# Performance work log

Measured on AMD Instinct MI355X. Metric: run time of the kernel, lower is better.

## Reference

```python
import jax, jax.numpy as jnp
import numpy as np

START_ID = 0  # vocab.wd_to_id['<START>']

B, T, V = 128, 256, 1000
C = H = E = 512          # context_size == hidden_size (hidden initialized to context)
IN = C + E               # LSTMCell input size


def setup_inputs() -> dict:
    key = jax.random.key(0)
    ks = jax.random.split(key, 10)
    s = 1.0 / np.sqrt(H)
    return {
        "context": jax.random.normal(ks[0], (B, C), dtype=jnp.float32),
        "target_tensor": jax.random.randint(ks[1], (B, T), 0, V),
        "coin": jax.random.uniform(ks[2], (T,), dtype=jnp.float32),
        "embed_table": jax.random.normal(ks[3], (V, E), dtype=jnp.float32) * 0.02,
        "W_ih": jax.random.uniform(ks[4], (4 * H, IN), dtype=jnp.float32, minval=-s, maxval=s),
        "W_hh": jax.random.uniform(ks[5], (4 * H, H), dtype=jnp.float32, minval=-s, maxval=s),
        "b_ih": jax.random.uniform(ks[6], (4 * H,), dtype=jnp.float32, minval=-s, maxval=s),
        "b_hh": jax.random.uniform(ks[7], (4 * H,), dtype=jnp.float32, minval=-s, maxval=s),
        "W_out": jax.random.uniform(ks[8], (V, H), dtype=jnp.float32, minval=-s, maxval=s),
        "b_out": jax.random.uniform(ks[9], (V,), dtype=jnp.float32, minval=-s, maxval=s),
    }


def reference(context, target_tensor, coin, embed_table, W_ih, W_hh, b_ih, b_hh, W_out, b_out):
    Bsz, Csz = context.shape
    Tlen = target_tensor.shape[1]
    Hsz = W_hh.shape[1]
    Vsz = W_out.shape[0]

    # teacher token for step i is target[:, i-1]; step 0 uses START
    prev_tok = jnp.concatenate(
        [jnp.full((Bsz, 1), START_ID, dtype=target_tensor.dtype), target_tensor[:, :-1]],
        axis=1,
    ).T  # (T, B)

    h0 = context                                   # hidden initialized to context
    c0 = jnp.zeros((Bsz, Hsz), dtype=context.dtype)
    logits0 = jnp.zeros((Bsz, Vsz), dtype=context.dtype)
    steps = jnp.arange(Tlen)

    def step(carry, xs):
        h, c, prev_logits = carry
        tok, r, i = xs
        greedy = jnp.argmax(prev_logits, axis=1)               # previous prediction
        idx = jnp.where(r > 0.5, tok, jnp.where(i == 0, START_ID, greedy))
        emb = embed_table[idx]                                 # (B, E)
        x = jnp.concatenate([context, emb], axis=1)            # (B, C+E)
        gates = x @ W_ih.T + b_ih + h @ W_hh.T + b_hh          # (B, 4H)
        ig, fg, gg, og = jnp.split(gates, 4, axis=1)           # torch order i,f,g,o
        c_new = jax.nn.sigmoid(fg) * c + jax.nn.sigmoid(ig) * jnp.tanh(gg)
        h_new = jax.nn.sigmoid(og) * jnp.tanh(c_new)
        logits = h_new @ W_out.T + b_out                       # (B, V)
        return (h_new, c_new, logits), logits

    (h, c, _), outs = jax.lax.scan(step, (h0, c0, logits0), (prev_tok, coin, steps))
    return outs.transpose(1, 0, 2), h, c  # (B, T, V), (B, H), (B, H)
```

## Files before the change

### kernel.cpp

```cpp
#include <hip/hip_runtime.h>
#include <cstdint>
#include <cstddef>

#define B_SZ 128
#define T_SZ 256
#define V_SZ 1000
#define H_SZ 512
#define NG   2048
#define VP   1024

typedef unsigned long long u64;

__device__ __forceinline__ unsigned fkey(float f) {
  unsigned u = __float_as_uint(f);
  return (u & 0x80000000u) ? ~u : (u | 0x80000000u);
}
__device__ __forceinline__ float sigf(float x) { return 1.0f / (1.0f + expf(-x)); }

__device__ __forceinline__ float aload(const float* p) {
  return __hip_atomic_load(p, __ATOMIC_RELAXED, __HIP_MEMORY_SCOPE_AGENT);
}
__device__ __forceinline__ float4 aload4(const float* p) {
  float4 r;
  r.x = __hip_atomic_load(p + 0, __ATOMIC_RELAXED, __HIP_MEMORY_SCOPE_AGENT);
  r.y = __hip_atomic_load(p + 1, __ATOMIC_RELAXED, __HIP_MEMORY_SCOPE_AGENT);
  r.z = __hip_atomic_load(p + 2, __ATOMIC_RELAXED, __HIP_MEMORY_SCOPE_AGENT);
  r.w = __hip_atomic_load(p + 3, __ATOMIC_RELAXED, __HIP_MEMORY_SCOPE_AGENT);
  return r;
}
__device__ __forceinline__ void astore(float* p, float v) {
  __hip_atomic_store(p, v, __ATOMIC_RELAXED, __HIP_MEMORY_SCOPE_AGENT);
}
__device__ __forceinline__ u64 aload64(const u64* p) {
  return __hip_atomic_load(p, __ATOMIC_RELAXED, __HIP_MEMORY_SCOPE_AGENT);
}
__device__ __forceinline__ void astore64(u64* p, u64 v) {
  __hip_atomic_store(p, v, __ATOMIC_RELAXED, __HIP_MEMORY_SCOPE_AGENT);
}

__device__ __forceinline__ void bcast_barrier(unsigned* arrive, unsigned gen) {
  __syncthreads();
  if (threadIdx.x == 0)
    __hip_atomic_store(arrive + blockIdx.x, gen, __ATOMIC_RELAXED, __HIP_MEMORY_SCOPE_AGENT);
  if (blockIdx.x == 0 && threadIdx.x < 64) {
    const int base = threadIdx.x * 4;
    for (;;) {
      bool ok = true;
#pragma unroll
      for (int j = 0; j < 4; ++j)
        ok &= (__hip_atomic_load(arrive + base + j, __ATOMIC_RELAXED,
                                 __HIP_MEMORY_SCOPE_AGENT) >= gen);
      if (__all(ok)) break;
      __builtin_amdgcn_s_sleep(2);
    }
    if (threadIdx.x == 0)
      __hip_atomic_store(arrive + 320, gen, __ATOMIC_RELAXED, __HIP_MEMORY_SCOPE_AGENT);
  }
  if (threadIdx.x == 0) {
    while (__hip_atomic_load(arrive + 320, __ATOMIC_RELAXED,
                             __HIP_MEMORY_SCOPE_AGENT) < gen)
      __builtin_amdgcn_s_sleep(2);
  }
  __syncthreads();
}


__global__ void k_transpose(const float* __restrict__ src, int srcLD, int col_off,
                            float* __restrict__ dst, int dstLD, int n_valid) {
  __shared__ float tile[32][33];
  const int tid = threadIdx.x;
  const int k0 = blockIdx.y * 32, n0 = blockIdx.x * 32;
  const int nl = tid >> 3, kq = (tid & 7) * 4;
  float4 v = make_float4(0.f, 0.f, 0.f, 0.f);
  if (n0 + nl < n_valid)
    v = *(const float4*)(src + (size_t)(n0 + nl) * srcLD + col_off + k0 + kq);
  tile[nl][kq + 0] = v.x; tile[nl][kq + 1] = v.y;
  tile[nl][kq + 2] = v.z; tile[nl][kq + 3] = v.w;
  __syncthreads();
  const int kl = tid >> 3, nq = (tid & 7) * 4;
  float4 o;
  o.x = tile[nq + 0][kl]; o.y = tile[nq + 1][kl];
  o.z = tile[nq + 2][kl]; o.w = tile[nq + 3][kl];
  *(float4*)(dst + (size_t)(k0 + kl) * dstLD + n0 + nq) = o;
}

__global__ void k_base(const float* __restrict__ ctx, const float* __restrict__ Wtc,
                       const float* __restrict__ b_ih, const float* __restrict__ b_hh,
                       float* __restrict__ base) {
  const int tid = threadIdx.x;
  const int n0 = blockIdx.x * 32, m0 = blockIdx.y * 32;
  const int ml = tid >> 3, ng = (tid & 7) * 4;
  const float* a = ctx + (size_t)(m0 + ml) * H_SZ;
  const float* b = Wtc + n0 + ng;
  float acc0 = 0.f, acc1 = 0.f, acc2 = 0.f, acc3 = 0.f;
#pragma unroll 4
  for (int k = 0; k < H_SZ; ++k) {
    float av = a[k];
    float4 bv = *(const float4*)(b + (size_t)k * NG);
    acc0 = fmaf(av, bv.x, acc0); acc1 = fmaf(av, bv.y, acc1);
    acc2 = fmaf(av, bv.z, acc2); acc3 = fmaf(av, bv.w, acc3);
  }
  const int n = n0 + ng;
  float* o = base + (size_t)(m0 + ml) * NG + n;
  o[0] = acc0 + b_ih[n + 0] + b_hh[n + 0];
  o[1] = acc1 + b_ih[n + 1] + b_hh[n + 1];
  o[2] = acc2 + b_ih[n + 2] + b_hh[n + 2];
  o[3] = acc3 + b_ih[n + 3] + b_hh[n + 3];
}

__global__ void k_init(const float* __restrict__ ctx, const float* __restrict__ b_out,
                       float* __restrict__ h0, float* __restrict__ bo,
                       unsigned* __restrict__ arrive) {
  const int i = blockIdx.x * 256 + threadIdx.x;
  h0[i] = ctx[i];
  if (i < VP) bo[i] = (i < V_SZ) ? b_out[i] : 0.f;
  if (i < 512) arrive[i] = 0u;
}

__global__ __launch_bounds__(512, 2) void k_persist(
    const float* __restrict__ Wt, const float* __restrict__ WoT,
    const float* __restrict__ base, const float* __restrict__ etbl,
    const float* __restrict__ coin, const int* __restrict__ tgt,
    const float* __restrict__ bo, float* __restrict__ h0buf, float* __restrict__ h1buf,
    float* __restrict__ out, u64* __restrict__ pk, unsigned* __restrict__ arrive) {
  __shared__ float smem[9216];
  __shared__ int idx_s[32];
  const int tid = threadIdx.x;
  const int bid = blockIdx.x;
  const int xcd = bid & 7, slot = bid >> 3;

  const int qt = xcd * 8 + (slot >> 2);
  const int mtA = slot & 3;
  const int q0 = qt * 8, m0A = mtA * 32;
  const int vt = xcd * 4 + (slot & 3);
  const int mtB = slot >> 2;
  const int n0B = vt * 32, m0B = mtB * 16;

  const int w = tid >> 6, lane = tid & 63;
  const int rg = lane >> 3, cg = lane & 7;
  float* As = smem + w * 1152;
  float* Bs = As + 576;
  const int kbA = w * 128;
  const int amA = lane >> 2, afA = (lane & 3) * 4;
  const int bkA = lane >> 3;
  const int bnA = (lane & 7) * 4;
  const int colA = (bnA >> 3) * 512 + q0 + (bnA & 7);
  float* As2 = smem + w * 896;
  float* Bs2 = As2 + 320;
  const int kbB = w * 64;
  const int amB = lane >> 2;

  const int mlc = tid >> 3, qlc = tid & 7;
  float bsr[4];
  size_t hIdx = 0;
  if (tid < 256) {
#pragma unroll
    for (int g = 0; g < 4; ++g)
      bsr[g] = base[(size_t)(m0A + mlc) * NG + g * 512 + q0 + qlc];
    hIdx = (size_t)(m0A + mlc) * H_SZ + q0 + qlc;
  }
  float creg = 0.f;

  const int mlb = tid >> 5, nlb = tid & 31;
  const int ngB = n0B + nlb, mgB = m0B + mlb;
  const float bor = bo[ngB];
  const size_t outBase = (size_t)mgB * ((size_t)T_SZ * V_SZ) + ngB;

#pragma unroll 1
  for (int t = 0; t < T_SZ; ++t) {
    const float* hRead  = (t & 1) ? h1buf : h0buf;
    float*       hWrite = (t & 1) ? h0buf : h1buf;

    if (tid < 32) {
      int id = 0;
      if (t > 0) {
        if (coin[t] > 0.5f) {
          id = tgt[(m0A + tid) * T_SZ + (t - 1)];
        } else {
          const u64* p = pk + (size_t)(m0A + tid) * 32;
          const unsigned tagw = (unsigned)((t - 1) & 0xFF);
          u64 best = 0ull;
#pragma unroll 1
          for (int q = 0; q < 32; ++q) {
            u64 v = aload64(p + q);
            while ((unsigned)(v & 0xFFu) != tagw) {
              __builtin_amdgcn_s_sleep(1);
              v = aload64(p + q);
            }
            best = (v > best) ? v : best;
          }
          id = 1023 - (int)((best >> 8) & 0x3FF);
        }
      }
      idx_s[tid] = id;
    }
    __syncthreads();

    {
      float acc[4][4];
#pragma unroll
      for (int i = 0; i < 4; ++i)
#pragma unroll
        for (int j = 0; j < 4; ++j) acc[i][j] = 0.f;

      float4 ra[2], rb[2];
      auto loadA = [&](int s, float4* r) {
        const int k = kbA + s * 16 + afA;
#pragma unroll
        for (int i = 0; i < 2; ++i) {
          const int m_ = amA + i * 16;
          if (k < 512)
            r[i] = *(const float4*)(etbl + (size_t)idx_s[m_] * 512 + k);
          else
            r[i] = aload4(hRead + (size_t)(m0A + m_) * H_SZ + (k - 512));
        }
      };
      auto loadB = [&](int s, float4* r) {
#pragma unroll
        for (int i = 0; i < 2; ++i)
          r[i] = *(const float4*)(Wt + (size_t)(kbA + s * 16 + bkA + i * 8) * NG + colA);
      };

      loadA(0, ra); loadB(0, rb);
#pragma unroll 1
      for (int s = 0; s < 8; ++s) {
#pragma unroll
        for (int i = 0; i < 2; ++i) {
          const int m_ = amA + i * 16;
          As[(afA + 0) * 36 + m_] = ra[i].x;
          As[(afA + 1) * 36 + m_] = ra[i].y;
          As[(afA + 2) * 36 + m_] = ra[i].z;
          As[(afA + 3) * 36 + m_] = ra[i].w;
          *(float4*)(Bs + (bkA + i * 8) * 36 + bnA) = rb[i];
        }
        float4 na[2], nb[2];
        if (s < 7) { loadA(s + 1, na); loadB(s + 1, nb); }
#pragma unroll
        for (int k = 0; k < 16; ++k) {
          float4 a = *(const float4*)(As + k * 36 + rg * 4);
          float4 b = *(const float4*)(Bs + k * 36 + cg * 4);
          acc[0][0] = fmaf(a.x, b.x, acc[0][0]); acc[0][1] = fmaf(a.x, b.y, acc[0][1]);
          acc[0][2] = fmaf(a.x, b.z, acc[0][2]); acc[0][3] = fmaf(a.x, b.w, acc[0][3]);
          acc[1][0] = fmaf(a.y, b.x, acc[1][0]); acc[1][1] = fmaf(a.y, b.y, acc[1][1]);
          acc[1][2] = fmaf(a.y, b.z, acc[1][2]); acc[1][3] = fmaf(a.y, b.w, acc[1][3]);
          acc[2][0] = fmaf(a.z, b.x, acc[2][0]); acc[2][1] = fmaf(a.z, b.y, acc[2][1]);
          acc[2][2] = fmaf(a.z, b.z, acc[2][2]); acc[2][3] = fmaf(a.z, b.w, acc[2][3]);
          acc[3][0] = fmaf(a.w, b.x, acc[3][0]); acc[3][1] = fmaf(a.w, b.y, acc[3][1]);
          acc[3][2] = fmaf(a.w, b.z, acc[3][2]); acc[3][3] = fmaf(a.w, b.w, acc[3][3]);
        }
        if (s < 7) { ra[0] = na[0]; ra[1] = na[1]; rb[0] = nb[0]; rb[1] = nb[1]; }
      }
      __syncthreads();
#pragma unroll
      for (int i = 0; i < 4; ++i)
#pragma unroll
        for (int j = 0; j < 4; ++j)
          smem[w * 1024 + (rg * 4 + i) * 32 + cg * 4 + j] = acc[i][j];
      __syncthreads();

      if (tid < 256) {
        float gv[4];
#pragma unroll
        for (int g = 0; g < 4; ++g) {
          float s_ = bsr[g];
          const int j = g * 8 + qlc;
#pragma unroll
          for (int w2 = 0; w2 < 8; ++w2) s_ += smem[w2 * 1024 + mlc * 32 + j];
          gv[g] = s_;
        }
        const float cn = sigf(gv[1]) * creg + sigf(gv[0]) * tanhf(gv[2]);
        creg = cn;
        astore(hWrite + hIdx, sigf(gv[3]) * tanhf(cn));
      }
    }
    bcast_barrier(arrive, (unsigned)(t + 1));

    {
      float acc[2][4];
#pragma unroll
      for (int i = 0; i < 2; ++i)
#pragma unroll
        for (int j = 0; j < 4; ++j) acc[i][j] = 0.f;

      float4 ra; float4 rb[2];
      auto loadA2 = [&](int s, float4& r) {
        r = aload4(hWrite + (size_t)(m0B + amB) * H_SZ + kbB + s * 16 + afA);
      };
      auto loadB2 = [&](int s, float4* r) {
#pragma unroll
        for (int i = 0; i < 2; ++i)
          r[i] = *(const float4*)(WoT + (size_t)(kbB + s * 16 + bkA + i * 8) * VP + n0B + bnA);
      };

      loadA2(0, ra); loadB2(0, rb);
#pragma unroll 1
      for (int s = 0; s < 4; ++s) {
        As2[(afA + 0) * 20 + amB] = ra.x;
        As2[(afA + 1) * 20 + amB] = ra.y;
        As2[(afA + 2) * 20 + amB] = ra.z;
        As2[(afA + 3) * 20 + amB] = ra.w;
#pragma unroll
        for (int i = 0; i < 2; ++i) *(float4*)(Bs2 + (bkA + i * 8) * 36 + bnA) = rb[i];
        float4 na; float4 nb[2];
        if (s < 3) { loadA2(s + 1, na); loadB2(s + 1, nb); }
#pragma unroll
        for (int k = 0; k < 16; ++k) {
          float2 a = *(const float2*)(As2 + k * 20 + rg * 2);
          float4 b = *(const float4*)(Bs2 + k * 36 + cg * 4);
          acc[0][0] = fmaf(a.x, b.x, acc[0][0]); acc[0][1] = fmaf(a.x, b.y, acc[0][1]);
          acc[0][2] = fmaf(a.x, b.z, acc[0][2]); acc[0][3] = fmaf(a.x, b.w, acc[0][3]);
          acc[1][0] = fmaf(a.y, b.x, acc[1][0]); acc[1][1] = fmaf(a.y, b.y, acc[1][1]);
          acc[1][2] = fmaf(a.y, b.z, acc[1][2]); acc[1][3] = fmaf(a.y, b.w, acc[1][3]);
        }
        if (s < 3) { ra = na; rb[0] = nb[0]; rb[1] = nb[1]; }
      }
      __syncthreads();
#pragma unroll
      for (int i = 0; i < 2; ++i)
#pragma unroll
        for (int j = 0; j < 4; ++j)
          smem[w * 512 + (rg * 2 + i) * 32 + cg * 4 + j] = acc[i][j];
      __syncthreads();

      float sres = bor;
#pragma unroll
      for (int w2 = 0; w2 < 8; ++w2) sres += smem[w2 * 512 + tid];
      u64 p = 0ull;
      if (ngB < V_SZ) {
        out[outBase + (size_t)t * V_SZ] = sres;
        p = ((u64)fkey(sres) << 32) | ((u64)(unsigned)(1023 - ngB) << 8)
            | (u64)(unsigned)(t & 0xFF);
      }
#pragma unroll
      for (int d = 16; d >= 1; d >>= 1) {
        u64 o = __shfl_xor(p, d, 64);
        p = (o > p) ? o : p;
      }
      if (nlb == 0) astore64(pk + (size_t)mgB * 32 + vt, p);
    }
  }

  const size_t off = (size_t)B_SZ * T_SZ * V_SZ;
  if (tid < 256) {
    out[off + (size_t)bid * 256 + tid] = aload(h0buf + (size_t)bid * 256 + tid);
    out[off + 65536 + hIdx] = creg;
  }
}

extern "C" void kernel_launch(void* const* d_in, const int* in_sizes, int n_in,
                              void* d_out, int out_size, void* d_ws, size_t ws_size,
                              hipStream_t stream) {
  (void)in_sizes; (void)n_in; (void)out_size; (void)ws_size;
  const float* ctx   = (const float*)d_in[0];
  const int*   tgt   = (const int*)d_in[1];
  const float* coin  = (const float*)d_in[2];
  const float* etbl  = (const float*)d_in[3];
  const float* W_ih  = (const float*)d_in[4];
  const float* W_hh  = (const float*)d_in[5];
  const float* b_ih  = (const float*)d_in[6];
  const float* b_hh  = (const float*)d_in[7];
  const float* W_out = (const float*)d_in[8];
  const float* b_out = (const float*)d_in[9];
  float* out = (float*)d_out;

  float* ws    = (float*)d_ws;
  float* Wt    = ws;
  float* Wtc   = Wt + 2097152;
  float* WoT   = Wtc + 1048576;
  float* base  = WoT + 524288;
  float* h0    = base + 262144;
  float* h1    = h0 + 65536;
  u64*   pk    = (u64*)(h1 + 65536);
  float* bo    = (float*)(pk + 4096);
  unsigned* arrive = (unsigned*)(bo + 1024);

  hipLaunchKernelGGL(k_transpose, dim3(64, 16), dim3(256), 0, stream,
                     W_ih, 1024, 512, Wt, NG, 2048);
  hipLaunchKernelGGL(k_transpose, dim3(64, 16), dim3(256), 0, stream,
                     W_hh, 512, 0, Wt + (size_t)512 * NG, NG, 2048);
  hipLaunchKernelGGL(k_transpose, dim3(64, 16), dim3(256), 0, stream,
                     W_ih, 1024, 0, Wtc, NG, 2048);
  hipLaunchKernelGGL(k_transpose, dim3(32, 16), dim3(256), 0, stream,
                     W_out, 512, 0, WoT, VP, 1000);
  hipLaunchKernelGGL(k_base, dim3(64, 4), dim3(256), 0, stream, ctx, Wtc, b_ih, b_hh, base);
  hipLaunchKernelGGL(k_init, dim3(256), dim3(256), 0, stream, ctx, b_out, h0, bo, arrive);

  void* args[] = { (void*)&Wt, (void*)&WoT, (void*)&base, (void*)&etbl, (void*)&coin,
                   (void*)&tgt, (void*)&bo, (void*)&h0, (void*)&h1, (void*)&out,
                   (void*)&pk, (void*)&arrive };
  hipLaunchCooperativeKernel((void*)k_persist, dim3(256), dim3(512), args, 0, stream);
}
```

Baseline: 10.26 ms.

## Partition persistent kernel into independent batch groups with local barriers

```diff
diff --git a/kernel.cpp b/kernel.cpp
--- a/kernel.cpp
+++ b/kernel.cpp
@@ -38,28 +38,18 @@
   __hip_atomic_store(p, v, __ATOMIC_RELAXED, __HIP_MEMORY_SCOPE_AGENT);
 }
 
-__device__ __forceinline__ void bcast_barrier(unsigned* arrive, unsigned gen) {
+__device__ __forceinline__ void group_barrier(unsigned* gflags, unsigned gen) {
   __syncthreads();
   if (threadIdx.x == 0)
-    __hip_atomic_store(arrive + blockIdx.x, gen, __ATOMIC_RELAXED, __HIP_MEMORY_SCOPE_AGENT);
-  if (blockIdx.x == 0 && threadIdx.x < 64) {
-    const int base = threadIdx.x * 4;
+    __hip_atomic_store(gflags + (blockIdx.x & 63), gen, __ATOMIC_RELAXED,
+                       __HIP_MEMORY_SCOPE_AGENT);
+  if (threadIdx.x < 64) {
     for (;;) {
-      bool ok = true;
-#pragma unroll
-      for (int j = 0; j < 4; ++j)
-        ok &= (__hip_atomic_load(arrive + base + j, __ATOMIC_RELAXED,
-                                 __HIP_MEMORY_SCOPE_AGENT) >= gen);
+      bool ok = (__hip_atomic_load(gflags + threadIdx.x, __ATOMIC_RELAXED,
+                                   __HIP_MEMORY_SCOPE_AGENT) >= gen);
       if (__all(ok)) break;
       __builtin_amdgcn_s_sleep(2);
     }
-    if (threadIdx.x == 0)
-      __hip_atomic_store(arrive + 320, gen, __ATOMIC_RELAXED, __HIP_MEMORY_SCOPE_AGENT);
-  }
-  if (threadIdx.x == 0) {
-    while (__hip_atomic_load(arrive + 320, __ATOMIC_RELAXED,
-                             __HIP_MEMORY_SCOPE_AGENT) < gen)
-      __builtin_amdgcn_s_sleep(2);
   }
   __syncthreads();
 }
@@ -127,14 +117,14 @@
   __shared__ int idx_s[32];
   const int tid = threadIdx.x;
   const int bid = blockIdx.x;
-  const int xcd = bid & 7, slot = bid >> 3;
-
-  const int qt = xcd * 8 + (slot >> 2);
-  const int mtA = slot & 3;
-  const int q0 = qt * 8, m0A = mtA * 32;
-  const int vt = xcd * 4 + (slot & 3);
-  const int mtB = slot >> 2;
-  const int n0B = vt * 32, m0B = mtB * 16;
+  const int grp = bid >> 6;
+  const int ls  = bid & 63;
+  unsigned* gflags = arrive + grp * 128;
+
+  const int q0 = ls * 8;
+  const int m0A = grp * 32;
+  const int vt = ls >> 1;
+  const int n0B = vt * 32, m0B = m0A + (ls & 1) * 16;
 
   const int w = tid >> 6, lane = tid & 63;
   const int rg = lane >> 3, cg = lane & 7;
@@ -273,7 +263,7 @@
         astore(hWrite + hIdx, sigf(gv[3]) * tanhf(cn));
       }
     }
-    bcast_barrier(arrive, (unsigned)(t + 1));
+    group_barrier(gflags, (unsigned)(t + 1));
 
     {
       float acc[2][4];
```

Result: slower. 10.67 ms (+4.0%).
